# Kernel optimization log

Measured on AMD Instinct MI355X. Metric: run time of the kernel, lower is better.

The kernel has to match this reference:

```python
import jax, jax.numpy as jnp
import numpy as np

N_NODES = 100_000
N_EDGES = 1_000_000
IN_CH = 32
EDGE_CH = 16
OUT_CH = 32
D_CAT = 2 * IN_CH + EDGE_CH  # 80
D_MID = 56                   # linspace(80, 32, 3)[1]


def setup_inputs() -> dict:
    key = jax.random.key(0)
    ks = jax.random.split(key, 8)
    x = jax.random.normal(ks[0], (N_NODES, IN_CH), dtype=jnp.float32)
    edge_index = jax.random.randint(ks[1], (2, N_EDGES), 0, N_NODES, dtype=jnp.int64)
    edge_attr = jax.random.normal(ks[2], (N_EDGES, EDGE_CH), dtype=jnp.float32)
    # MLP params: Linear(80->56), Linear(56->32), bias=True (homogeneous_flag=False)
    W1 = jax.random.normal(ks[3], (D_CAT, D_MID), dtype=jnp.float32) / np.sqrt(D_CAT).astype(np.float32)
    b1 = jnp.zeros((D_MID,), dtype=jnp.float32)
    W2 = jax.random.normal(ks[4], (D_MID, OUT_CH), dtype=jnp.float32) / np.sqrt(D_MID).astype(np.float32)
    b2 = jnp.zeros((OUT_CH,), dtype=jnp.float32)
    return {"x": x, "edge_index": edge_index, "edge_attr": edge_attr,
            "W1": W1, "b1": b1, "W2": W2, "b2": b2}


def reference(x, edge_index, edge_attr, W1, b1, W2, b2):
    num_nodes = x.shape[0]
    rol, col = edge_index[0], edge_index[1]
    # gather node pairs + concat edge features: [E, 2*in + edge]
    e = jnp.concatenate([x[rol], x[col], edge_attr], axis=-1)
    # edge MLP (LeakyReLU after every layer, as in IterGNN's MLP)
    h = jax.nn.leaky_relu(e @ W1 + b1)
    v = jax.nn.leaky_relu(h @ W2 + b2)  # [E, out]
    # Max aggregation by destination node (scatter-max); empty segments -> 0
    agg = jax.ops.segment_max(v, col, num_segments=num_nodes)
    agg = jnp.where(jnp.isneginf(agg), jnp.zeros((), dtype=agg.dtype), agg)
    # elementwise max with trailing slice of input features
    out = jnp.maximum(agg, x[:, -v.shape[-1]:])
    return out
```

## Files before the change

kernel.cpp:

```cpp
#include <hip/hip_runtime.h>

#define N_NODES 100000
#define IN_CH 32
#define EDGE_CH 16
#define OUT_CH 32
#define D_CAT 80
#define D_MID 56

#define BKT_SHIFT 6
#define BKT_NODES 64
#define NB 1563
#define NB_ALL 1568
#define CAP 1024

#define NSUP 196
#define CAP_SUP 5632
#define K1_EDGES 4096
#define K2_ITERS 11

#define EPB 128
#define W1F_SH 6144
#define W2F_SH 2048
#define WIMG_SH (W1F_SH + W2F_SH)
#define FEATF_SH 12288
#define HF_SH 8192

#define AGG_LD 33
#define ENC_NEGINF 0x007FFFFFu

typedef short short8 __attribute__((ext_vector_type(8)));
typedef float f32x4 __attribute__((ext_vector_type(4)));
typedef int i32x2 __attribute__((ext_vector_type(2)));

#define WS_IMG    0
#define WS_B1     16384
#define WS_B2     16640
#define WS_SUPCNT 16768
#define WS_GCNT   17664
#define WS_SUPREC 24576
#define WS_REC    8855552
#define WS_NEED_A (WS_REC + (size_t)NB_ALL * CAP * 8)
#define WS_NEED_B (24576 + (size_t)NB_ALL * CAP * 8)

__device__ __forceinline__ unsigned fenc(float f) {
    unsigned u = __float_as_uint(f);
    return (u & 0x80000000u) ? ~u : (u | 0x80000000u);
}
__device__ __forceinline__ float fdec(unsigned u) {
    u = (u & 0x80000000u) ? (u ^ 0x80000000u) : ~u;
    return __uint_as_float(u);
}
__device__ __forceinline__ float bfr(float f) {
    unsigned u = __float_as_uint(f);
    u = (u + 0x7FFFu + ((u >> 16) & 1u)) & 0xFFFF0000u;
    return __uint_as_float(u);
}
__device__ __forceinline__ unsigned short bf16b(float f) {
    unsigned u = __float_as_uint(f);
    return (unsigned short)((u + 0x7FFFu + ((u >> 16) & 1u)) >> 16);
}

__device__ void build_weight_image(const float* __restrict__ W1, const float* __restrict__ b1,
                                   const float* __restrict__ W2, const float* __restrict__ b2,
                                   unsigned short* __restrict__ wsImg,
                                   float* __restrict__ wsb1, float* __restrict__ wsb2,
                                   int t, int nthr) {
    for (int s = t; s < W1F_SH; s += nthr) {
        int j = s & 7, l = (s >> 3) & 63, fi = s >> 9;
        int nt = fi & 3, ks = fi >> 2;
        int l15 = l & 15, quad = l >> 4;
        int n = nt * 16 + l15, k = ks * 32 + quad * 8 + j;
        wsImg[s] = (n < D_MID && k < D_CAT) ? bf16b(W1[k * D_MID + n]) : (unsigned short)0;
    }
    for (int s = t; s < W2F_SH; s += nthr) {
        int j = s & 7, l = (s >> 3) & 63, fi = s >> 9;
        int nt = fi & 1, ks = fi >> 1;
        int l15 = l & 15, quad = l >> 4;
        int n = nt * 16 + l15, k = ks * 32 + quad * 8 + j;
        wsImg[W1F_SH + s] = (k < D_MID) ? bf16b(W2[k * OUT_CH + n]) : (unsigned short)0;
    }
    if (t < 64) wsb1[t] = (t < D_MID) ? bfr(b1[t]) : 0.f;
    else if (t < 96) wsb2[t - 64] = bfr(b2[t - 64]);
}

__global__ __launch_bounds__(512) void coarse_bin(
    const int* __restrict__ ei, int nE, int* __restrict__ gSupCnt, int2* __restrict__ supRec,
    const float* __restrict__ W1, const float* __restrict__ b1,
    const float* __restrict__ W2, const float* __restrict__ b2,
    unsigned short* __restrict__ wsImg, float* __restrict__ wsb1, float* __restrict__ wsb2)
{
    __shared__ int2 staged[K1_EDGES];
    __shared__ int cnt[256], sc[256], cur[256], wb[256];
    const int t = threadIdx.x;
    if (blockIdx.x == 0) build_weight_image(W1, b1, W2, b2, wsImg, wsb1, wsb2, t, 512);
    if (t < 256) cnt[t] = 0;
    __syncthreads();

    const int lo = blockIdx.x * K1_EDGES;
    int rdst[8], rsrc[8];
#pragma unroll
    for (int k = 0; k < 8; ++k) {
        int e = lo + k * 512 + t;
        bool v = e < nE;
        rdst[k] = v ? __builtin_nontemporal_load(ei + nE + e) : -1;
        rsrc[k] = v ? __builtin_nontemporal_load(ei + e) : 0;
        if ((unsigned)rdst[k] >= N_NODES) rdst[k] = -1;
        if ((unsigned)rsrc[k] >= N_NODES) rsrc[k] = 0;
        if (rdst[k] >= 0) atomicAdd(&cnt[rdst[k] >> 9], 1);
    }
    __syncthreads();
    if (t < 256) sc[t] = cnt[t];
    __syncthreads();
    for (int off = 1; off < 256; off <<= 1) {
        int v = 0;
        if (t < 256 && t >= off) v = sc[t - off];
        __syncthreads();
        if (t < 256) sc[t] += v;
        __syncthreads();
    }
    if (t < NSUP) {
        int c = cnt[t];
        int excl = sc[t] - c;
        int g = c ? atomicAdd(&gSupCnt[t], c) : 0;
        wb[t] = t * CAP_SUP + g - excl;
        cur[t] = excl;
    }
    __syncthreads();
#pragma unroll
    for (int k = 0; k < 8; ++k) {
        if (rdst[k] >= 0) {
            int s = rdst[k] >> 9;
            int pos = atomicAdd(&cur[s], 1);
            int e = lo + k * 512 + t;
            staged[pos] = make_int2(rsrc[k] | (s << 24), ((rdst[k] & 511) << 20) | e);
        }
    }
    __syncthreads();
    int nv = sc[NSUP - 1];
    for (int i = t; i < nv; i += 512) {
        int2 r = staged[i];
        int s = (unsigned)r.x >> 24;
        int addr = wb[s] + i;
        if (addr - s * CAP_SUP < CAP_SUP)
            supRec[addr] = make_int2(r.x & 0x00FFFFFF, r.y);
    }
}

__global__ __launch_bounds__(512) void fine_bin(
    const int* __restrict__ gSupCnt, const int2* __restrict__ supRec,
    int* __restrict__ gCnt, int2* __restrict__ rec)
{
    __shared__ int2 staged[CAP_SUP];
    __shared__ int c8[8], ex8[8], cur8[8];
    const int s = blockIdx.x, t = threadIdx.x;
    const int cntS = min(gSupCnt[s], CAP_SUP);
    if (t < 8) c8[t] = 0;
    __syncthreads();
    int2 r[K2_ITERS];
#pragma unroll
    for (int k = 0; k < K2_ITERS; ++k) {
        int i = k * 512 + t;
        r[k] = (i < cntS) ? supRec[(size_t)s * CAP_SUP + i] : make_int2(0, 0);
        if (i < cntS) atomicAdd(&c8[(r[k].y >> 26) & 7], 1);
    }
    __syncthreads();
    if (t == 0) {
        int a = 0;
        for (int f = 0; f < 8; ++f) { ex8[f] = a; cur8[f] = a; a += c8[f]; }
    }
    __syncthreads();
#pragma unroll
    for (int k = 0; k < K2_ITERS; ++k) {
        int i = k * 512 + t;
        if (i < cntS) {
            int f = (r[k].y >> 26) & 7;
            int pos = atomicAdd(&cur8[f], 1);
            staged[pos] = make_int2(r[k].x | (f << 24),
                                    (((r[k].y >> 20) & 63) << 20) | (r[k].y & 0xFFFFF));
        }
    }
    __syncthreads();
    for (int i = t; i < cntS; i += 512) {
        int2 v = staged[i];
        int f = (unsigned)v.x >> 24;
        int loc = i - ex8[f];
        if (loc < CAP)
            rec[(size_t)(s * 8 + f) * CAP + loc] = make_int2(v.x & 0x00FFFFFF, v.y);
    }
    if (t < 8) gCnt[s * 8 + t] = min(c8[t], CAP);
}

__global__ __launch_bounds__(512) void scatter_append(
    const int* __restrict__ ei, int* __restrict__ gCnt, int2* __restrict__ rec, int nE,
    const float* __restrict__ W1, const float* __restrict__ b1,
    const float* __restrict__ W2, const float* __restrict__ b2,
    unsigned short* __restrict__ wsImg, float* __restrict__ wsb1, float* __restrict__ wsb2)
{
    __shared__ int lh[NB];
    __shared__ int lbase[NB];
    if (blockIdx.x == 0) build_weight_image(W1, b1, W2, b2, wsImg, wsb1, wsb2, threadIdx.x, 512);
    for (int i = threadIdx.x; i < NB; i += 512) lh[i] = 0;
    __syncthreads();
    int per = (nE + gridDim.x - 1) / gridDim.x;
    int lo = blockIdx.x * per;
    int hi = min(lo + per, nE);
    for (int e = lo + threadIdx.x; e < hi; e += 512) {
        int dst = __builtin_nontemporal_load(ei + nE + e);
        if ((unsigned)dst < N_NODES) atomicAdd(&lh[dst >> BKT_SHIFT], 1);
    }
    __syncthreads();
    for (int i = threadIdx.x; i < NB; i += 512) {
        int c = lh[i];
        lbase[i] = c ? atomicAdd(&gCnt[i], c) : 0;
        lh[i] = 0;
    }
    __syncthreads();
    for (int e = lo + threadIdx.x; e < hi; e += 512) {
        int dst = __builtin_nontemporal_load(ei + nE + e);
        if ((unsigned)dst >= N_NODES) continue;
        int b = dst >> BKT_SHIFT;
        int p = lbase[b] + atomicAdd(&lh[b], 1);
        if (p >= CAP) continue;
        int src = __builtin_nontemporal_load(ei + e);
        if ((unsigned)src >= N_NODES) src = 0;
        rec[(size_t)b * CAP + p] = make_int2(src, ((dst & (BKT_NODES - 1)) << 20) | e);
    }
}

__global__ __launch_bounds__(512, 6) void bucket_mlp(
    const float* __restrict__ x, const float* __restrict__ ea,
    const int2* __restrict__ rec, const int* __restrict__ gCnt,
    const unsigned short* __restrict__ wsImg,
    const float* __restrict__ wsb1, const float* __restrict__ wsb2,
    float* __restrict__ out)
{
    __shared__ unsigned short sFeatF[FEATF_SH];
    __shared__ unsigned short sWgt[WIMG_SH];
    __shared__ unsigned aggL[BKT_NODES * AGG_LD];
    __shared__ float sb1f[64];
    __shared__ float sb2f[32];
    __shared__ int sdl[EPB];

    unsigned short* const sW1F = sWgt;
    unsigned short* const sW2F = sWgt + W1F_SH;
    unsigned short* const sHF  = sFeatF;

    const int t = threadIdx.x;
    const int nodeBase = blockIdx.x << BKT_SHIFT;
    const int base = blockIdx.x * CAP;
    const int cnt  = min(gCnt[blockIdx.x], CAP);

    for (int i = t; i < WIMG_SH / 8; i += 512)
        *(short8*)&sWgt[i * 8] = *(const short8*)(wsImg + i * 8);
    for (int i = t; i < BKT_NODES * AGG_LD; i += 512) aggL[i] = ENC_NEGINF;
    if (t < 64) sb1f[t] = wsb1[t];
    else if (t < 96) sb2f[t - 64] = wsb2[t - 64];

    const int wave = t >> 6;
    const int l15  = t & 15;
    const int quad = (t & 63) >> 4;
    const int wm   = wave * 16;
    const int lane = t & 63;
    const int slot = t >> 2, q = t & 3;
    const int sl15 = slot & 15, swave = slot >> 4;

    float4 rv[6];
    int rdl;

    auto loadChunk = [&](int c0e) {
        int idx = c0e + slot;
        bool ok = idx < cnt;
        i32x2 r2 = ok ? *(const i32x2*)(rec + base + idx) : (i32x2){0, 0};
        rdl = ok ? ((r2.y >> 20) & 63) : -1;
        int e = r2.y & 0xFFFFF;
        int src = r2.x;
        int dn = nodeBase + ((r2.y >> 20) & 63);
        const float* xs = x + (size_t)src * IN_CH;
        const float* xd = x + (size_t)dn * IN_CH;
        const float* ep = ea + (size_t)e * EDGE_CH;
        float4 z = make_float4(0, 0, 0, 0);
#pragma unroll
        for (int k = 0; k < 3; ++k) {
            int cj = 3 * q + k;
            const float* p = nullptr;
            if (cj < 4) p = xs + cj * 8;
            else if (cj < 8) p = xd + (cj - 4) * 8;
            else if (cj < 10) p = ep + (cj - 8) * 8;
            if (ok && p) { rv[2 * k] = ((const float4*)p)[0]; rv[2 * k + 1] = ((const float4*)p)[1]; }
            else { rv[2 * k] = z; rv[2 * k + 1] = z; }
        }
    };
    auto storeChunk = [&]() {
        if (q == 0) sdl[slot] = rdl;
#pragma unroll
        for (int k = 0; k < 3; ++k) {
            int cj = 3 * q + k;
            float4 a = rv[2 * k], b = rv[2 * k + 1];
            short8 p8 = { (short)bf16b(a.x), (short)bf16b(a.y), (short)bf16b(a.z), (short)bf16b(a.w),
                          (short)bf16b(b.x), (short)bf16b(b.y), (short)bf16b(b.z), (short)bf16b(b.w) };
            int a16 = (swave * 3 + (cj >> 2)) * 64 + (cj & 3) * 16 + sl15;
            *(short8*)&sFeatF[a16 * 8] = p8;
        }
    };

    loadChunk(0);
    for (int c0e = 0; c0e < cnt; c0e += EPB) {
        storeChunk();
        __syncthreads();
        loadChunk(c0e + EPB);

        f32x4 acc[4];
#pragma unroll
        for (int nt = 0; nt < 4; ++nt) acc[nt] = (f32x4){0.f, 0.f, 0.f, 0.f};
#pragma unroll
        for (int ks = 0; ks < 3; ++ks) {
            short8 bfrag = *(const short8*)&sFeatF[((wave * 3 + ks) * 64 + lane) * 8];
#pragma unroll
            for (int nt = 0; nt < 4; ++nt) {
                short8 afrag = *(const short8*)&sW1F[((ks * 4 + nt) * 64 + lane) * 8];
                acc[nt] = __builtin_amdgcn_mfma_f32_16x16x32_bf16(afrag, bfrag, acc[nt], 0, 0, 0);
            }
        }
        __syncthreads();

        {
#pragma unroll
            for (int nt = 0; nt < 4; ++nt) {
                int c0 = nt * 16 + quad * 4;
                int ks2 = nt >> 1;
                int quad2 = (nt * 2 + (quad >> 1)) & 3;
                int off = (quad & 1) * 4;
                ushort4 p;
#pragma unroll
                for (int j = 0; j < 4; ++j) {
                    float v = acc[nt][j] + sb1f[c0 + j];
                    v = (v > 0.f) ? v : 0.01f * v;
                    ((unsigned short*)&p)[j] = (c0 + j < D_MID) ? bf16b(v) : (unsigned short)0;
                }
                *(ushort4*)&sHF[((wave * 2 + ks2) * 64 + quad2 * 16 + l15) * 8 + off] = p;
            }
        }
        __syncthreads();

        f32x4 acc2[2];
#pragma unroll
        for (int nt = 0; nt < 2; ++nt) acc2[nt] = (f32x4){0.f, 0.f, 0.f, 0.f};
#pragma unroll
        for (int ks = 0; ks < 2; ++ks) {
            short8 bfrag = *(const short8*)&sHF[((wave * 2 + ks) * 64 + lane) * 8];
#pragma unroll
            for (int nt = 0; nt < 2; ++nt) {
                short8 afrag = *(const short8*)&sW2F[((ks * 2 + nt) * 64 + lane) * 8];
                acc2[nt] = __builtin_amdgcn_mfma_f32_16x16x32_bf16(afrag, bfrag, acc2[nt], 0, 0, 0);
            }
        }

        {
            int dl = sdl[wm + l15];
            if (dl >= 0) {
                unsigned* arow = &aggL[dl * AGG_LD];
#pragma unroll
                for (int nt = 0; nt < 2; ++nt) {
                    int c0 = nt * 16 + quad * 4;
#pragma unroll
                    for (int j = 0; j < 4; ++j) {
                        float v = acc2[nt][j] + sb2f[c0 + j];
                        v = (v > 0.f) ? v : 0.01f * v;
                        atomicMax(arow + c0 + j, fenc(bfr(v)));
                    }
                }
            }
        }
        __syncthreads();
    }
    __syncthreads();

    {
        int nl = t >> 3, g4 = t & 7;
        int node = nodeBase + nl;
        if (node < N_NODES) {
            float4 xv = ((const float4*)(x + (size_t)node * IN_CH))[g4];
            const unsigned* ar = &aggL[nl * AGG_LD + g4 * 4];
            float4 o;
            o.x = fmaxf((ar[0] == ENC_NEGINF) ? 0.f : fdec(ar[0]), bfr(xv.x));
            o.y = fmaxf((ar[1] == ENC_NEGINF) ? 0.f : fdec(ar[1]), bfr(xv.y));
            o.z = fmaxf((ar[2] == ENC_NEGINF) ? 0.f : fdec(ar[2]), bfr(xv.z));
            o.w = fmaxf((ar[3] == ENC_NEGINF) ? 0.f : fdec(ar[3]), bfr(xv.w));
            ((float4*)(out + (size_t)node * OUT_CH))[g4] = o;
        }
    }
}

extern "C" void kernel_launch(void* const* d_in, const int* in_sizes, int n_in,
                              void* d_out, int out_size, void* d_ws, size_t ws_size,
                              hipStream_t stream) {
    const float* x  = (const float*)d_in[0];
    const int*   ei = (const int*)d_in[1];
    const float* ea = (const float*)d_in[2];
    const float* W1 = (const float*)d_in[3];
    const float* b1 = (const float*)d_in[4];
    const float* W2 = (const float*)d_in[5];
    const float* b2 = (const float*)d_in[6];

    char* ws = (char*)d_ws;
    unsigned short* wsImg = (unsigned short*)(ws + WS_IMG);
    float* wsb1 = (float*)(ws + WS_B1);
    float* wsb2 = (float*)(ws + WS_B2);
    int* gSupCnt = (int*)(ws + WS_SUPCNT);
    int* gCnt = (int*)(ws + WS_GCNT);

    const int nE = in_sizes[1] / 2;
    float* out = (float*)d_out;

    if (ws_size >= WS_NEED_A) {
        int2* supRec = (int2*)(ws + WS_SUPREC);
        int2* rec    = (int2*)(ws + WS_REC);
        hipMemsetAsync(gSupCnt, 0, NSUP * sizeof(int), stream);
        coarse_bin<<<(nE + K1_EDGES - 1) / K1_EDGES, 512, 0, stream>>>(
            ei, nE, gSupCnt, supRec, W1, b1, W2, b2, wsImg, wsb1, wsb2);
        fine_bin<<<NSUP, 512, 0, stream>>>(gSupCnt, supRec, gCnt, rec);
        bucket_mlp<<<NB, 512, 0, stream>>>(x, ea, rec, gCnt, wsImg, wsb1, wsb2, out);
    } else {
        int2* rec = (int2*)(ws + 24576);
        hipMemsetAsync(gCnt, 0, NB_ALL * sizeof(int), stream);
        scatter_append<<<128, 512, 0, stream>>>(ei, gCnt, rec, nE, W1, b1, W2, b2, wsImg, wsb1, wsb2);
        bucket_mlp<<<NB, 512, 0, stream>>>(x, ea, rec, gCnt, wsImg, wsb1, wsb2, out);
    }
}
```

Baseline: 210.1 us.

## Pre-convert node features to bf16 and use ballot-based fine binning

Adds a pass, folded into the binning kernels, that converts x to a bf16 copy in workspace. The edge MLP kernel then gathers source and destination features at half the bytes and skips per-edge conversion. fine_bin is also rewritten to place records with wave ballots and per-bucket atomics, dropping the shared staging buffer and two barriers. The costs are extra workspace, a full pass over x, and a record order within each bucket that is no longer deterministic.

```diff
diff --git a/kernel.cpp b/kernel.cpp
--- a/kernel.cpp
+++ b/kernel.cpp
@@ -39,8 +39,13 @@
 #define WS_GCNT   17664
 #define WS_SUPREC 24576
 #define WS_REC    8855552
-#define WS_NEED_A (WS_REC + (size_t)NB_ALL * CAP * 8)
-#define WS_NEED_B (24576 + (size_t)NB_ALL * CAP * 8)
+#define WS_XB_A   21700608
+#define XB_BYTES  6400000
+#define WS_NEED_A ((size_t)WS_XB_A)
+#define WS_NEED_AX ((size_t)WS_XB_A + XB_BYTES)
+#define WS_XB_B   12869632
+#define WS_NEED_B ((size_t)WS_XB_B)
+#define WS_NEED_BX ((size_t)WS_XB_B + XB_BYTES)
 
 __device__ __forceinline__ unsigned fenc(float f) {
     unsigned u = __float_as_uint(f);
@@ -58,6 +63,19 @@
 __device__ __forceinline__ unsigned short bf16b(float f) {
     unsigned u = __float_as_uint(f);
     return (unsigned short)((u + 0x7FFFu + ((u >> 16) & 1u)) >> 16);
+}
+
+__device__ __forceinline__ void convert_x_bf16(const float* __restrict__ x,
+                                               unsigned short* __restrict__ xb,
+                                               int gtid, int gstride) {
+    const int tot = N_NODES * IN_CH / 8;
+    for (int i = gtid; i < tot; i += gstride) {
+        float4 a = ((const float4*)x)[2 * i];
+        float4 b = ((const float4*)x)[2 * i + 1];
+        short8 p = { (short)bf16b(a.x), (short)bf16b(a.y), (short)bf16b(a.z), (short)bf16b(a.w),
+                     (short)bf16b(b.x), (short)bf16b(b.y), (short)bf16b(b.z), (short)bf16b(b.w) };
+        *(short8*)&xb[i * 8] = p;
+    }
 }
 
 __device__ void build_weight_image(const float* __restrict__ W1, const float* __restrict__ b1,
@@ -148,57 +166,60 @@
 
 __global__ __launch_bounds__(512) void fine_bin(
     const int* __restrict__ gSupCnt, const int2* __restrict__ supRec,
-    int* __restrict__ gCnt, int2* __restrict__ rec)
+    int* __restrict__ gCnt, int2* __restrict__ rec,
+    const float* __restrict__ x, unsigned short* __restrict__ xb)
 {
-    __shared__ int2 staged[CAP_SUP];
-    __shared__ int c8[8], ex8[8], cur8[8];
+    __shared__ int cur8[8];
     const int s = blockIdx.x, t = threadIdx.x;
+    const int lane = t & 63;
+
+    if (xb) convert_x_bf16(x, xb, s * 512 + t, NSUP * 512);
+
     const int cntS = min(gSupCnt[s], CAP_SUP);
-    if (t < 8) c8[t] = 0;
-    __syncthreads();
+    if (t < 8) cur8[t] = 0;
+    __syncthreads();
+
     int2 r[K2_ITERS];
 #pragma unroll
     for (int k = 0; k < K2_ITERS; ++k) {
         int i = k * 512 + t;
         r[k] = (i < cntS) ? supRec[(size_t)s * CAP_SUP + i] : make_int2(0, 0);
-        if (i < cntS) atomicAdd(&c8[(r[k].y >> 26) & 7], 1);
-    }
-    __syncthreads();
-    if (t == 0) {
-        int a = 0;
-        for (int f = 0; f < 8; ++f) { ex8[f] = a; cur8[f] = a; a += c8[f]; }
-    }
-    __syncthreads();
+    }
 #pragma unroll
     for (int k = 0; k < K2_ITERS; ++k) {
         int i = k * 512 + t;
-        if (i < cntS) {
-            int f = (r[k].y >> 26) & 7;
-            int pos = atomicAdd(&cur8[f], 1);
-            staged[pos] = make_int2(r[k].x | (f << 24),
-                                    (((r[k].y >> 20) & 63) << 20) | (r[k].y & 0xFFFFF));
-        }
-    }
-    __syncthreads();
-    for (int i = t; i < cntS; i += 512) {
-        int2 v = staged[i];
-        int f = (unsigned)v.x >> 24;
-        int loc = i - ex8[f];
-        if (loc < CAP)
-            rec[(size_t)(s * 8 + f) * CAP + loc] = make_int2(v.x & 0x00FFFFFF, v.y);
-    }
-    if (t < 8) gCnt[s * 8 + t] = min(c8[t], CAP);
+        bool v = i < cntS;
+        int f = v ? ((r[k].y >> 26) & 7) : -1;
+        int rank = 0, wbase = 0;
+#pragma unroll
+        for (int vv = 0; vv < 8; ++vv) {
+            unsigned long long m = __ballot(f == vv);
+            if (lane == vv) wbase = m ? atomicAdd(&cur8[vv], (int)__popcll(m)) : 0;
+            if (f == vv) rank = (int)__popcll(m & ((1ull << lane) - 1ull));
+        }
+        int base = __shfl(wbase, f & 7);
+        if (v) {
+            int pos = base + rank;
+            if (pos < CAP)
+                rec[(size_t)(s * 8 + f) * CAP + pos] =
+                    make_int2(r[k].x, (((r[k].y >> 20) & 63) << 20) | (r[k].y & 0xFFFFF));
+        }
+    }
+    __syncthreads();
+    if (t < 8) gCnt[s * 8 + t] = min(cur8[t], CAP);
 }
 
 __global__ __launch_bounds__(512) void scatter_append(
     const int* __restrict__ ei, int* __restrict__ gCnt, int2* __restrict__ rec, int nE,
     const float* __restrict__ W1, const float* __restrict__ b1,
     const float* __restrict__ W2, const float* __restrict__ b2,
-    unsigned short* __restrict__ wsImg, float* __restrict__ wsb1, float* __restrict__ wsb2)
+    unsigned short* __restrict__ wsImg, float* __restrict__ wsb1, float* __restrict__ wsb2,
+    const float* __restrict__ x, unsigned short* __restrict__ xb)
 {
     __shared__ int lh[NB];
     __shared__ int lbase[NB];
     if (blockIdx.x == 0) build_weight_image(W1, b1, W2, b2, wsImg, wsb1, wsb2, threadIdx.x, 512);
+    if (xb) convert_x_bf16(x, xb, blockIdx.x * 512 + threadIdx.x, gridDim.x * 512);
     for (int i = threadIdx.x; i < NB; i += 512) lh[i] = 0;
     __syncthreads();
     int per = (nE + gridDim.x - 1) / gridDim.x;
@@ -227,8 +248,10 @@
     }
 }
 
+template<int XB>
 __global__ __launch_bounds__(512, 6) void bucket_mlp(
-    const float* __restrict__ x, const float* __restrict__ ea,
+    const float* __restrict__ x, const unsigned short* __restrict__ xb,
+    const float* __restrict__ ea,
     const int2* __restrict__ rec, const int* __restrict__ gCnt,
     const unsigned short* __restrict__ wsImg,
     const float* __restrict__ wsb1, const float* __restrict__ wsb2,
@@ -265,6 +288,7 @@
     const int sl15 = slot & 15, swave = slot >> 4;
 
     float4 rv[6];
+    short8 rv16[3];
     int rdl;
 
     auto loadChunk = [&](int c0e) {
@@ -275,19 +299,41 @@
         int e = r2.y & 0xFFFFF;
         int src = r2.x;
         int dn = nodeBase + ((r2.y >> 20) & 63);
-        const float* xs = x + (size_t)src * IN_CH;
-        const float* xd = x + (size_t)dn * IN_CH;
-        const float* ep = ea + (size_t)e * EDGE_CH;
-        float4 z = make_float4(0, 0, 0, 0);
-#pragma unroll
-        for (int k = 0; k < 3; ++k) {
-            int cj = 3 * q + k;
-            const float* p = nullptr;
-            if (cj < 4) p = xs + cj * 8;
-            else if (cj < 8) p = xd + (cj - 4) * 8;
-            else if (cj < 10) p = ep + (cj - 8) * 8;
-            if (ok && p) { rv[2 * k] = ((const float4*)p)[0]; rv[2 * k + 1] = ((const float4*)p)[1]; }
-            else { rv[2 * k] = z; rv[2 * k + 1] = z; }
+        if constexpr (XB) {
+            const short8* xs8 = (const short8*)(xb + (size_t)src * IN_CH);
+            const short8* xd8 = (const short8*)(xb + (size_t)dn * IN_CH);
+            const float* ep = ea + (size_t)e * EDGE_CH;
+#pragma unroll
+            for (int k = 0; k < 3; ++k) {
+                int cj = 3 * q + k;
+                short8 pv = {0, 0, 0, 0, 0, 0, 0, 0};
+                if (ok) {
+                    if (cj < 4) pv = xs8[cj];
+                    else if (cj < 8) pv = xd8[cj - 4];
+                    else if (cj < 10) {
+                        float4 a = ((const float4*)ep)[(cj - 8) * 2];
+                        float4 b = ((const float4*)ep)[(cj - 8) * 2 + 1];
+                        pv = short8{ (short)bf16b(a.x), (short)bf16b(a.y), (short)bf16b(a.z), (short)bf16b(a.w),
+                                     (short)bf16b(b.x), (short)bf16b(b.y), (short)bf16b(b.z), (short)bf16b(b.w) };
+                    }
+                }
+                rv16[k] = pv;
+            }
+        } else {
+            const float* xs = x + (size_t)src * IN_CH;
+            const float* xd = x + (size_t)dn * IN_CH;
+            const float* ep = ea + (size_t)e * EDGE_CH;
+            float4 z = make_float4(0, 0, 0, 0);
+#pragma unroll
+            for (int k = 0; k < 3; ++k) {
+                int cj = 3 * q + k;
+                const float* p = nullptr;
+                if (cj < 4) p = xs + cj * 8;
+                else if (cj < 8) p = xd + (cj - 4) * 8;
+                else if (cj < 10) p = ep + (cj - 8) * 8;
+                if (ok && p) { rv[2 * k] = ((const float4*)p)[0]; rv[2 * k + 1] = ((const float4*)p)[1]; }
+                else { rv[2 * k] = z; rv[2 * k + 1] = z; }
+            }
         }
     };
     auto storeChunk = [&]() {
@@ -295,9 +341,14 @@
 #pragma unroll
         for (int k = 0; k < 3; ++k) {
             int cj = 3 * q + k;
-            float4 a = rv[2 * k], b = rv[2 * k + 1];
-            short8 p8 = { (short)bf16b(a.x), (short)bf16b(a.y), (short)bf16b(a.z), (short)bf16b(a.w),
-                          (short)bf16b(b.x), (short)bf16b(b.y), (short)bf16b(b.z), (short)bf16b(b.w) };
+            short8 p8;
+            if constexpr (XB) {
+                p8 = rv16[k];
+            } else {
+                float4 a = rv[2 * k], b = rv[2 * k + 1];
+                p8 = short8{ (short)bf16b(a.x), (short)bf16b(a.y), (short)bf16b(a.z), (short)bf16b(a.w),
+                             (short)bf16b(b.x), (short)bf16b(b.y), (short)bf16b(b.z), (short)bf16b(b.w) };
+            }
             int a16 = (swave * 3 + (cj >> 2)) * 64 + (cj & 3) * 16 + sl15;
             *(short8*)&sFeatF[a16 * 8] = p8;
         }
@@ -379,13 +430,21 @@
         int nl = t >> 3, g4 = t & 7;
         int node = nodeBase + nl;
         if (node < N_NODES) {
-            float4 xv = ((const float4*)(x + (size_t)node * IN_CH))[g4];
             const unsigned* ar = &aggL[nl * AGG_LD + g4 * 4];
             float4 o;
-            o.x = fmaxf((ar[0] == ENC_NEGINF) ? 0.f : fdec(ar[0]), bfr(xv.x));
-            o.y = fmaxf((ar[1] == ENC_NEGINF) ? 0.f : fdec(ar[1]), bfr(xv.y));
-            o.z = fmaxf((ar[2] == ENC_NEGINF) ? 0.f : fdec(ar[2]), bfr(xv.z));
-            o.w = fmaxf((ar[3] == ENC_NEGINF) ? 0.f : fdec(ar[3]), bfr(xv.w));
+            if constexpr (XB) {
+                ushort4 xw = ((const ushort4*)(xb + (size_t)node * IN_CH))[g4];
+                o.x = fmaxf((ar[0] == ENC_NEGINF) ? 0.f : fdec(ar[0]), __uint_as_float((unsigned)xw.x << 16));
+                o.y = fmaxf((ar[1] == ENC_NEGINF) ? 0.f : fdec(ar[1]), __uint_as_float((unsigned)xw.y << 16));
+                o.z = fmaxf((ar[2] == ENC_NEGINF) ? 0.f : fdec(ar[2]), __uint_as_float((unsigned)xw.z << 16));
+                o.w = fmaxf((ar[3] == ENC_NEGINF) ? 0.f : fdec(ar[3]), __uint_as_float((unsigned)xw.w << 16));
+            } else {
+                float4 xv = ((const float4*)(x + (size_t)node * IN_CH))[g4];
+                o.x = fmaxf((ar[0] == ENC_NEGINF) ? 0.f : fdec(ar[0]), bfr(xv.x));
+                o.y = fmaxf((ar[1] == ENC_NEGINF) ? 0.f : fdec(ar[1]), bfr(xv.y));
+                o.z = fmaxf((ar[2] == ENC_NEGINF) ? 0.f : fdec(ar[2]), bfr(xv.z));
+                o.w = fmaxf((ar[3] == ENC_NEGINF) ? 0.f : fdec(ar[3]), bfr(xv.w));
+            }
             ((float4*)(out + (size_t)node * OUT_CH))[g4] = o;
         }
     }
@@ -415,15 +474,26 @@
     if (ws_size >= WS_NEED_A) {
         int2* supRec = (int2*)(ws + WS_SUPREC);
         int2* rec    = (int2*)(ws + WS_REC);
+        bool xbOn = ws_size >= WS_NEED_AX;
+        unsigned short* xb = xbOn ? (unsigned short*)(ws + WS_XB_A) : nullptr;
         hipMemsetAsync(gSupCnt, 0, NSUP * sizeof(int), stream);
         coarse_bin<<<(nE + K1_EDGES - 1) / K1_EDGES, 512, 0, stream>>>(
             ei, nE, gSupCnt, supRec, W1, b1, W2, b2, wsImg, wsb1, wsb2);
-        fine_bin<<<NSUP, 512, 0, stream>>>(gSupCnt, supRec, gCnt, rec);
-        bucket_mlp<<<NB, 512, 0, stream>>>(x, ea, rec, gCnt, wsImg, wsb1, wsb2, out);
+        fine_bin<<<NSUP, 512, 0, stream>>>(gSupCnt, supRec, gCnt, rec, x, xb);
+        if (xbOn)
+            bucket_mlp<1><<<NB, 512, 0, stream>>>(x, xb, ea, rec, gCnt, wsImg, wsb1, wsb2, out);
+        else
+            bucket_mlp<0><<<NB, 512, 0, stream>>>(x, nullptr, ea, rec, gCnt, wsImg, wsb1, wsb2, out);
     } else {
         int2* rec = (int2*)(ws + 24576);
+        bool xbOn = ws_size >= WS_NEED_BX;
+        unsigned short* xb = xbOn ? (unsigned short*)(ws + WS_XB_B) : nullptr;
         hipMemsetAsync(gCnt, 0, NB_ALL * sizeof(int), stream);
-        scatter_append<<<128, 512, 0, stream>>>(ei, gCnt, rec, nE, W1, b1, W2, b2, wsImg, wsb1, wsb2);
-        bucket_mlp<<<NB, 512, 0, stream>>>(x, ea, rec, gCnt, wsImg, wsb1, wsb2, out);
-    }
-}
+        scatter_append<<<128, 512, 0, stream>>>(ei, gCnt, rec, nE, W1, b1, W2, b2,
+                                                wsImg, wsb1, wsb2, x, xb);
+        if (xbOn)
+            bucket_mlp<1><<<NB, 512, 0, stream>>>(x, xb, ea, rec, gCnt, wsImg, wsb1, wsb2, out);
+        else
+            bucket_mlp<0><<<NB, 512, 0, stream>>>(x, nullptr, ea, rec, gCnt, wsImg, wsb1, wsb2, out);
+    }
+}
```

Result: slower. 227.2 us (+8.1%).
